# Kernel optimization log

Measured on AMD Instinct MI355X. Metric: run time of the kernel, lower is better.

Reference implementation:

```python
import jax, jax.numpy as jnp
import numpy as np

N_SRC = 50000   # nodes of src type
N_TRG = 50000   # nodes of trg type
H = 256         # hidden_size
E = 300000      # number of labeled edges for this message type


def setup_inputs() -> dict:
    key = jax.random.key(0)
    k0, k1, k2, k3 = jax.random.split(key, 4)
    x_src = jax.random.normal(k0, (N_SRC, H), dtype=jnp.float32)
    x_trg = jax.random.normal(k1, (N_TRG, H), dtype=jnp.float32)
    # nn.Parameter(torch.rand(H, H) * 0.01)
    R = jax.random.uniform(k2, (H, H), dtype=jnp.float32) * 0.01
    edge_index = jax.random.randint(k3, (2, E), 0, N_SRC, dtype=jnp.int64)
    return {"x_src": x_src, "x_trg": x_trg, "R": R, "edge_index": edge_index}


def reference(x_src, x_trg, R, edge_index):
    # Gather per-edge endpoint embeddings (index_select on dim 0).
    nodes_left = x_src[edge_index[0]]    # (E, H)
    nodes_right = x_trg[edge_index[1]]   # (E, H)
    # Original: sum((nodes_right @ R) @ nodes_left.T, dim=-1)
    # == (nodes_right @ R) @ nodes_left.sum(0)  -- same math, avoids the E x E
    # intermediate which is infeasible to materialize at this scale.
    left_sum = nodes_left.sum(axis=0)    # (H,)
    scores = (nodes_right @ R) @ left_sum  # (E,)
    return scores
```

## Files before the change

### kernel.cpp

```cpp
#include <hip/hip_runtime.h>

#define HDIM 256
#define CSB  512
#define RSTRIDE (CSB * 4)

__global__ void k_zero(uint4* __restrict__ p, int n4) {
    int i = blockIdx.x * blockDim.x + threadIdx.x;
    if (i < n4) p[i] = make_uint4(0u, 0u, 0u, 0u);
}

__global__ void k_count(const int4* __restrict__ src4, const int* __restrict__ src,
                        int E, unsigned int* __restrict__ cnt) {
    int i = blockIdx.x * blockDim.x + threadIdx.x;
    int E4 = E >> 2;
    if (i < E4) {
        int4 v = src4[i];
        atomicAdd(&cnt[v.x], 1u); atomicAdd(&cnt[v.y], 1u);
        atomicAdd(&cnt[v.z], 1u); atomicAdd(&cnt[v.w], 1u);
    }
    if (i < (E & 3)) atomicAdd(&cnt[src[(E4 << 2) + i]], 1u);
}

__global__ __launch_bounds__(256)
void k_colsum(const float4* __restrict__ xs4,
              const unsigned int* __restrict__ cnt,
              int Ns, float* __restrict__ pT) {
    const int colgrp = threadIdx.x & 63;
    const int rowOff = threadIdx.x >> 6;
    const int bid = blockIdx.x;
    float4 acc = make_float4(0.f, 0.f, 0.f, 0.f);

    for (int n = bid * 4 + rowOff; n < Ns; n += 8 * RSTRIDE) {
        float  c[8];
        float4 x[8];
        #pragma unroll
        for (int j = 0; j < 8; ++j) {
            int r = n + j * RSTRIDE;
            c[j] = 0.f;
            x[j] = make_float4(0.f, 0.f, 0.f, 0.f);
            if (r < Ns) {
                c[j] = (float)cnt[r];
                x[j] = xs4[(size_t)r * 64 + colgrp];
            }
        }
        #pragma unroll
        for (int j = 0; j < 8; ++j) {
            acc.x += c[j] * x[j].x; acc.y += c[j] * x[j].y;
            acc.z += c[j] * x[j].z; acc.w += c[j] * x[j].w;
        }
    }

    __shared__ float s[4 * HDIM];
    const int col = colgrp * 4;
    s[rowOff * HDIM + col + 0] = acc.x;
    s[rowOff * HDIM + col + 1] = acc.y;
    s[rowOff * HDIM + col + 2] = acc.z;
    s[rowOff * HDIM + col + 3] = acc.w;
    __syncthreads();
    const int tid = threadIdx.x;
    float part = (s[tid] + s[HDIM + tid]) + (s[2 * HDIM + tid] + s[3 * HDIM + tid]);
    pT[(size_t)tid * CSB + bid] = part;
}

__global__ __launch_bounds__(256)
void k_reduceT(const float* __restrict__ pT, float* __restrict__ ls) {
    const int h = blockIdx.x;
    const int tid = threadIdx.x;
    const float* row = pT + (size_t)h * CSB;
    float a = row[tid] + row[tid + 256];
    #pragma unroll
    for (int o = 32; o > 0; o >>= 1) a += __shfl_down(a, o, 64);
    __shared__ float s[4];
    if ((tid & 63) == 0) s[tid >> 6] = a;
    __syncthreads();
    if (tid == 0) ls[h] = (s[0] + s[1]) + (s[2] + s[3]);
}

__global__ __launch_bounds__(256)
void k_matvec(const float* __restrict__ Rm, const float* __restrict__ ls,
              float* __restrict__ v) {
    __shared__ float lss[HDIM];
    const int i = threadIdx.x;
    lss[i] = ls[i];
    __syncthreads();
    const float4* R4 = (const float4*)(Rm + (size_t)i * HDIM);
    float acc = 0.f;
    #pragma unroll
    for (int j = 0; j < 64; ++j) {
        float4 r = R4[j];
        acc += r.x * lss[4 * j] + r.y * lss[4 * j + 1] + r.z * lss[4 * j + 2] + r.w * lss[4 * j + 3];
    }
    v[i] = acc;
}

__global__ __launch_bounds__(256)
void k_rowdot(const float4* __restrict__ xt4, const float* __restrict__ v,
              int N, float* __restrict__ t) {
    const int lane = threadIdx.x & 63;
    const float4 vr = ((const float4*)v)[lane];
    const int nw = (gridDim.x * blockDim.x) >> 6;
    const int n0 = (blockIdx.x * blockDim.x + threadIdx.x) >> 6;

    for (int n = n0; n < N; n += 4 * nw) {
        float d[4] = {0.f, 0.f, 0.f, 0.f};
        #pragma unroll
        for (int j = 0; j < 4; ++j) {
            int r = n + j * nw;
            if (r < N) {
                float4 x = xt4[(size_t)r * 64 + lane];
                d[j] = x.x * vr.x + x.y * vr.y + x.z * vr.z + x.w * vr.w;
            }
        }
        #pragma unroll
        for (int o = 32; o > 0; o >>= 1) {
            #pragma unroll
            for (int j = 0; j < 4; ++j) d[j] += __shfl_down(d[j], o, 64);
        }
        if (lane == 0) {
            #pragma unroll
            for (int j = 0; j < 4; ++j) {
                int r = n + j * nw;
                if (r < N) t[r] = d[j];
            }
        }
    }
}

__global__ void k_gather(const int4* __restrict__ trg4, const int* __restrict__ trg, int E,
                         const float* __restrict__ t,
                         float4* __restrict__ out4, float* __restrict__ out) {
    int i = blockIdx.x * blockDim.x + threadIdx.x;
    int E4 = E >> 2;
    if (i < E4) {
        int4 v = trg4[i];
        out4[i] = make_float4(t[v.x], t[v.y], t[v.z], t[v.w]);
    }
    if (i < (E & 3)) {
        int e = (E4 << 2) + i;
        out[e] = t[trg[e]];
    }
}

extern "C" void kernel_launch(void* const* d_in, const int* in_sizes, int n_in,
                              void* d_out, int out_size, void* d_ws, size_t ws_size,
                              hipStream_t stream) {
    const float* x_src = (const float*)d_in[0];
    const float* x_trg = (const float*)d_in[1];
    const float* Rm    = (const float*)d_in[2];
    const int*   edge  = (const int*)d_in[3];
    float* out = (float*)d_out;

    const int Ns = in_sizes[0] / HDIM;
    const int Nt = in_sizes[1] / HDIM;
    const int E  = in_sizes[3] / 2;

    char* ws = (char*)d_ws;
    size_t off = 0;
    auto alloc = [&](size_t bytes) -> void* {
        void* p = ws + off;
        off = (off + bytes + 255) & ~(size_t)255;
        return p;
    };
    unsigned int* cnt = (unsigned int*)alloc((size_t)Ns * sizeof(unsigned int));
    float* pT = (float*)alloc((size_t)HDIM * CSB * sizeof(float));
    float* ls = (float*)alloc(HDIM * sizeof(float));
    float* v  = (float*)alloc(HDIM * sizeof(float));
    float* t  = (float*)alloc((size_t)Nt * sizeof(float));
    (void)ws_size; (void)n_in; (void)out_size;

    const int n4 = (Ns + 3) / 4;
    k_zero<<<(n4 + 255) / 256, 256, 0, stream>>>((uint4*)cnt, n4);

    const int E4 = E >> 2;
    const int cntThreads = (E4 > 0 ? E4 : 1);
    k_count<<<(cntThreads + 255) / 256, 256, 0, stream>>>(
        (const int4*)edge, edge, E, cnt);

    k_colsum<<<CSB, 256, 0, stream>>>((const float4*)x_src, cnt, Ns, pT);

    k_reduceT<<<HDIM, 256, 0, stream>>>(pT, ls);

    k_matvec<<<1, 256, 0, stream>>>(Rm, ls, v);

    k_rowdot<<<1024, 256, 0, stream>>>((const float4*)x_trg, v, Nt, t);

    k_gather<<<(cntThreads + 255) / 256, 256, 0, stream>>>(
        (const int4*)(edge + E), edge + E, E, t, (float4*)out, out);
}
```

Baseline: 61.42 us.

## Software-pipeline colsum/rowdot loads and fuse reduction with matvec

The column-sum and row-dot kernels now prefetch the next four rows into registers while computing on the current four, so memory loads overlap with arithmetic. The column-sum grid grows from 512 to 1024 blocks. The separate transpose-reduce and matvec kernels are merged into one 1024-thread block, which removes a launch and the intermediate ls buffer. The costs are higher register pressure from the double-buffered loads and a single-block reduction over a larger partial-sum array.

```diff
diff --git a/kernel.cpp b/kernel.cpp
--- a/kernel.cpp
+++ b/kernel.cpp
@@ -1,8 +1,8 @@
 #include <hip/hip_runtime.h>
 
 #define HDIM 256
-#define CSB  512
-#define RSTRIDE (CSB * 4)
+#define CSB  1024
+#define RDB  1024
 
 __global__ void k_zero(uint4* __restrict__ p, int n4) {
     int i = blockIdx.x * blockDim.x + threadIdx.x;
@@ -22,36 +22,47 @@
 }
 
 __global__ __launch_bounds__(256)
-void k_colsum(const float4* __restrict__ xs4,
-              const unsigned int* __restrict__ cnt,
+void k_colsum(const float4* __restrict__ xs4, const unsigned int* __restrict__ cnt,
               int Ns, float* __restrict__ pT) {
-    const int colgrp = threadIdx.x & 63;
+    const int lane = threadIdx.x & 63;
+    const int wv = blockIdx.x * 4 + (threadIdx.x >> 6);
+    const int NW = CSB * 4;
+    float4 acc = make_float4(0.f, 0.f, 0.f, 0.f);
+
+    float c0 = 0.f, c1 = 0.f, c2 = 0.f, c3 = 0.f;
+    float4 x0 = make_float4(0,0,0,0), x1 = x0, x2 = x0, x3 = x0;
+    int r = wv;
+    if (r          < Ns) { c0 = (float)cnt[r];          x0 = xs4[(size_t)r * 64 + lane]; }
+    if (r + NW     < Ns) { c1 = (float)cnt[r + NW];     x1 = xs4[(size_t)(r + NW) * 64 + lane]; }
+    if (r + 2 * NW < Ns) { c2 = (float)cnt[r + 2 * NW]; x2 = xs4[(size_t)(r + 2 * NW) * 64 + lane]; }
+    if (r + 3 * NW < Ns) { c3 = (float)cnt[r + 3 * NW]; x3 = xs4[(size_t)(r + 3 * NW) * 64 + lane]; }
+
+    for (; r + 7 * NW < Ns; r += 4 * NW) {
+        const int p = r + 4 * NW;
+        float  nc0 = (float)cnt[p];           float4 nx0 = xs4[(size_t)p * 64 + lane];
+        float  nc1 = (float)cnt[p + NW];      float4 nx1 = xs4[(size_t)(p + NW) * 64 + lane];
+        float  nc2 = (float)cnt[p + 2 * NW];  float4 nx2 = xs4[(size_t)(p + 2 * NW) * 64 + lane];
+        float  nc3 = (float)cnt[p + 3 * NW];  float4 nx3 = xs4[(size_t)(p + 3 * NW) * 64 + lane];
+        acc.x += c0 * x0.x; acc.y += c0 * x0.y; acc.z += c0 * x0.z; acc.w += c0 * x0.w;
+        acc.x += c1 * x1.x; acc.y += c1 * x1.y; acc.z += c1 * x1.z; acc.w += c1 * x1.w;
+        acc.x += c2 * x2.x; acc.y += c2 * x2.y; acc.z += c2 * x2.z; acc.w += c2 * x2.w;
+        acc.x += c3 * x3.x; acc.y += c3 * x3.y; acc.z += c3 * x3.z; acc.w += c3 * x3.w;
+        c0 = nc0; x0 = nx0; c1 = nc1; x1 = nx1;
+        c2 = nc2; x2 = nx2; c3 = nc3; x3 = nx3;
+    }
+    acc.x += c0 * x0.x; acc.y += c0 * x0.y; acc.z += c0 * x0.z; acc.w += c0 * x0.w;
+    acc.x += c1 * x1.x; acc.y += c1 * x1.y; acc.z += c1 * x1.z; acc.w += c1 * x1.w;
+    acc.x += c2 * x2.x; acc.y += c2 * x2.y; acc.z += c2 * x2.z; acc.w += c2 * x2.w;
+    acc.x += c3 * x3.x; acc.y += c3 * x3.y; acc.z += c3 * x3.z; acc.w += c3 * x3.w;
+    for (int s = r + 4 * NW; s < Ns; s += NW) {
+        float  cc = (float)cnt[s];
+        float4 xx = xs4[(size_t)s * 64 + lane];
+        acc.x += cc * xx.x; acc.y += cc * xx.y; acc.z += cc * xx.z; acc.w += cc * xx.w;
+    }
+
+    __shared__ float s[4 * HDIM];
+    const int col = lane * 4;
     const int rowOff = threadIdx.x >> 6;
-    const int bid = blockIdx.x;
-    float4 acc = make_float4(0.f, 0.f, 0.f, 0.f);
-
-    for (int n = bid * 4 + rowOff; n < Ns; n += 8 * RSTRIDE) {
-        float  c[8];
-        float4 x[8];
-        #pragma unroll
-        for (int j = 0; j < 8; ++j) {
-            int r = n + j * RSTRIDE;
-            c[j] = 0.f;
-            x[j] = make_float4(0.f, 0.f, 0.f, 0.f);
-            if (r < Ns) {
-                c[j] = (float)cnt[r];
-                x[j] = xs4[(size_t)r * 64 + colgrp];
-            }
-        }
-        #pragma unroll
-        for (int j = 0; j < 8; ++j) {
-            acc.x += c[j] * x[j].x; acc.y += c[j] * x[j].y;
-            acc.z += c[j] * x[j].z; acc.w += c[j] * x[j].w;
-        }
-    }
-
-    __shared__ float s[4 * HDIM];
-    const int col = colgrp * 4;
     s[rowOff * HDIM + col + 0] = acc.x;
     s[rowOff * HDIM + col + 1] = acc.y;
     s[rowOff * HDIM + col + 2] = acc.z;
@@ -59,38 +70,45 @@
     __syncthreads();
     const int tid = threadIdx.x;
     float part = (s[tid] + s[HDIM + tid]) + (s[2 * HDIM + tid] + s[3 * HDIM + tid]);
-    pT[(size_t)tid * CSB + bid] = part;
-}
-
-__global__ __launch_bounds__(256)
-void k_reduceT(const float* __restrict__ pT, float* __restrict__ ls) {
-    const int h = blockIdx.x;
+    pT[(size_t)tid * CSB + blockIdx.x] = part;
+}
+
+__global__ __launch_bounds__(1024)
+void k_reduce_mv(const float4* __restrict__ pT4, const float* __restrict__ Rm,
+                 float* __restrict__ v) {
     const int tid = threadIdx.x;
-    const float* row = pT + (size_t)h * CSB;
-    float a = row[tid] + row[tid + 256];
+    const int h = tid >> 2;
+    const int q = tid & 3;
+    __shared__ float red[4][HDIM];
+    __shared__ float lss[HDIM];
+
+    const float4* row = pT4 + (size_t)h * (CSB / 4) + q * (CSB / 16);
+    float4 s4 = make_float4(0.f, 0.f, 0.f, 0.f);
     #pragma unroll
-    for (int o = 32; o > 0; o >>= 1) a += __shfl_down(a, o, 64);
-    __shared__ float s[4];
-    if ((tid & 63) == 0) s[tid >> 6] = a;
-    __syncthreads();
-    if (tid == 0) ls[h] = (s[0] + s[1]) + (s[2] + s[3]);
-}
-
-__global__ __launch_bounds__(256)
-void k_matvec(const float* __restrict__ Rm, const float* __restrict__ ls,
-              float* __restrict__ v) {
-    __shared__ float lss[HDIM];
-    const int i = threadIdx.x;
-    lss[i] = ls[i];
-    __syncthreads();
-    const float4* R4 = (const float4*)(Rm + (size_t)i * HDIM);
-    float acc = 0.f;
+    for (int i0 = 0; i0 < CSB / 16; i0 += 8) {
+        float4 t0 = row[i0 + 0], t1 = row[i0 + 1], t2 = row[i0 + 2], t3 = row[i0 + 3];
+        float4 t4 = row[i0 + 4], t5 = row[i0 + 5], t6 = row[i0 + 6], t7 = row[i0 + 7];
+        s4.x += t0.x + t4.x; s4.y += t0.y + t4.y; s4.z += t0.z + t4.z; s4.w += t0.w + t4.w;
+        s4.x += t1.x + t5.x; s4.y += t1.y + t5.y; s4.z += t1.z + t5.z; s4.w += t1.w + t5.w;
+        s4.x += t2.x + t6.x; s4.y += t2.y + t6.y; s4.z += t2.z + t6.z; s4.w += t2.w + t6.w;
+        s4.x += t3.x + t7.x; s4.y += t3.y + t7.y; s4.z += t3.z + t7.z; s4.w += t3.w + t7.w;
+    }
+    red[q][h] = (s4.x + s4.y) + (s4.z + s4.w);
+    __syncthreads();
+    if (tid < HDIM) lss[tid] = (red[0][tid] + red[1][tid]) + (red[2][tid] + red[3][tid]);
+    __syncthreads();
+
+    const float4* R4 = (const float4*)Rm + (size_t)h * 64 + q * 16;
+    float m = 0.f;
     #pragma unroll
-    for (int j = 0; j < 64; ++j) {
-        float4 r = R4[j];
-        acc += r.x * lss[4 * j] + r.y * lss[4 * j + 1] + r.z * lss[4 * j + 2] + r.w * lss[4 * j + 3];
-    }
-    v[i] = acc;
+    for (int j = 0; j < 16; ++j) {
+        float4 rr = R4[j];
+        const int b = q * 64 + j * 4;
+        m += rr.x * lss[b] + rr.y * lss[b + 1] + rr.z * lss[b + 2] + rr.w * lss[b + 3];
+    }
+    red[q][h] = m;
+    __syncthreads();
+    if (tid < HDIM) v[tid] = (red[0][tid] + red[1][tid]) + (red[2][tid] + red[3][tid]);
 }
 
 __global__ __launch_bounds__(256)
@@ -98,32 +116,54 @@
               int N, float* __restrict__ t) {
     const int lane = threadIdx.x & 63;
     const float4 vr = ((const float4*)v)[lane];
-    const int nw = (gridDim.x * blockDim.x) >> 6;
-    const int n0 = (blockIdx.x * blockDim.x + threadIdx.x) >> 6;
-
-    for (int n = n0; n < N; n += 4 * nw) {
-        float d[4] = {0.f, 0.f, 0.f, 0.f};
-        #pragma unroll
-        for (int j = 0; j < 4; ++j) {
-            int r = n + j * nw;
-            if (r < N) {
-                float4 x = xt4[(size_t)r * 64 + lane];
-                d[j] = x.x * vr.x + x.y * vr.y + x.z * vr.z + x.w * vr.w;
-            }
-        }
+    const int wv = blockIdx.x * 4 + (threadIdx.x >> 6);
+    const int NW = RDB * 4;
+
+    float4 x0 = make_float4(0,0,0,0), x1 = x0, x2 = x0, x3 = x0;
+    int r = wv;
+    if (r          < N) x0 = xt4[(size_t)r * 64 + lane];
+    if (r + NW     < N) x1 = xt4[(size_t)(r + NW) * 64 + lane];
+    if (r + 2 * NW < N) x2 = xt4[(size_t)(r + 2 * NW) * 64 + lane];
+    if (r + 3 * NW < N) x3 = xt4[(size_t)(r + 3 * NW) * 64 + lane];
+
+#define RD_DOT(X) ((X).x * vr.x + (X).y * vr.y + (X).z * vr.z + (X).w * vr.w)
+    for (; r + 7 * NW < N; r += 4 * NW) {
+        const int p = r + 4 * NW;
+        float4 nx0 = xt4[(size_t)p * 64 + lane];
+        float4 nx1 = xt4[(size_t)(p + NW) * 64 + lane];
+        float4 nx2 = xt4[(size_t)(p + 2 * NW) * 64 + lane];
+        float4 nx3 = xt4[(size_t)(p + 3 * NW) * 64 + lane];
+        float d0 = RD_DOT(x0), d1 = RD_DOT(x1), d2 = RD_DOT(x2), d3 = RD_DOT(x3);
         #pragma unroll
         for (int o = 32; o > 0; o >>= 1) {
-            #pragma unroll
-            for (int j = 0; j < 4; ++j) d[j] += __shfl_down(d[j], o, 64);
+            d0 += __shfl_down(d0, o, 64); d1 += __shfl_down(d1, o, 64);
+            d2 += __shfl_down(d2, o, 64); d3 += __shfl_down(d3, o, 64);
+        }
+        if (lane == 0) { t[r] = d0; t[r + NW] = d1; t[r + 2 * NW] = d2; t[r + 3 * NW] = d3; }
+        x0 = nx0; x1 = nx1; x2 = nx2; x3 = nx3;
+    }
+    {
+        float d0 = RD_DOT(x0), d1 = RD_DOT(x1), d2 = RD_DOT(x2), d3 = RD_DOT(x3);
+        #pragma unroll
+        for (int o = 32; o > 0; o >>= 1) {
+            d0 += __shfl_down(d0, o, 64); d1 += __shfl_down(d1, o, 64);
+            d2 += __shfl_down(d2, o, 64); d3 += __shfl_down(d3, o, 64);
         }
         if (lane == 0) {
-            #pragma unroll
-            for (int j = 0; j < 4; ++j) {
-                int r = n + j * nw;
-                if (r < N) t[r] = d[j];
-            }
+            if (r          < N) t[r]          = d0;
+            if (r + NW     < N) t[r + NW]     = d1;
+            if (r + 2 * NW < N) t[r + 2 * NW] = d2;
+            if (r + 3 * NW < N) t[r + 3 * NW] = d3;
         }
     }
+    for (int s = r + 4 * NW; s < N; s += NW) {
+        float4 xx = xt4[(size_t)s * 64 + lane];
+        float d = RD_DOT(xx);
+        #pragma unroll
+        for (int o = 32; o > 0; o >>= 1) d += __shfl_down(d, o, 64);
+        if (lane == 0) t[s] = d;
+    }
+#undef RD_DOT
 }
 
 __global__ void k_gather(const int4* __restrict__ trg4, const int* __restrict__ trg, int E,
@@ -163,7 +203,6 @@
     };
     unsigned int* cnt = (unsigned int*)alloc((size_t)Ns * sizeof(unsigned int));
     float* pT = (float*)alloc((size_t)HDIM * CSB * sizeof(float));
-    float* ls = (float*)alloc(HDIM * sizeof(float));
     float* v  = (float*)alloc(HDIM * sizeof(float));
     float* t  = (float*)alloc((size_t)Nt * sizeof(float));
     (void)ws_size; (void)n_in; (void)out_size;
@@ -178,11 +217,9 @@
 
     k_colsum<<<CSB, 256, 0, stream>>>((const float4*)x_src, cnt, Ns, pT);
 
-    k_reduceT<<<HDIM, 256, 0, stream>>>(pT, ls);
-
-    k_matvec<<<1, 256, 0, stream>>>(Rm, ls, v);
-
-    k_rowdot<<<1024, 256, 0, stream>>>((const float4*)x_trg, v, Nt, t);
+    k_reduce_mv<<<1, 1024, 0, stream>>>((const float4*)pT, Rm, v);
+
+    k_rowdot<<<RDB, 256, 0, stream>>>((const float4*)x_trg, v, Nt, t);
 
     k_gather<<<(cntThreads + 255) / 256, 256, 0, stream>>>(
         (const int4*)(edge + E), edge + E, E, t, (float4*)out, out);
```

Result: slower. 97.37 us (+58.5%).
